# Kernel optimization log

Measured on AMD Instinct MI355X. Metric: run time of the kernel, lower is better.

## Reference

```python
import jax, jax.numpy as jnp
import numpy as np

K = 9            # kernel_size * dilation
ALPHA = 0.2      # LeakyReLU slope in GAT attention
LRELU = 0.01     # Grapher.layer1 default LeakyReLU slope
EPS_NORM = 1e-12
BN_EPS = 1e-5
NEG_INF = -9e15


def setup_inputs() -> dict:
    key = jax.random.key(0)
    ks = jax.random.split(key, 9)
    B, C, H, W = 16, 64, 32, 32
    nheads, nhid = 4, 15
    return {
        "x": jax.random.normal(ks[0], (B, C, H, W), jnp.float32),
        "W_heads": jax.random.normal(ks[1], (nheads, C, nhid), jnp.float32) * 0.2,
        "a_heads": jax.random.normal(ks[2], (nheads, 2 * nhid, 1), jnp.float32) * 0.2,
        "W_out": jax.random.normal(ks[3], (nheads * nhid, C), jnp.float32) * 0.2,
        "a_out": jax.random.normal(ks[4], (2 * C, 1), jnp.float32) * 0.2,
        "conv_w": jax.random.normal(ks[5], (C, C), jnp.float32) * 0.1,
        "conv_b": jax.random.normal(ks[6], (C,), jnp.float32) * 0.1,
        "bn_gamma": jnp.ones((C,), jnp.float32),
        "bn_beta": jnp.zeros((C,), jnp.float32),
    }


def _gat_layer(h, adj, W, a, concat):
    # h: [B,N,Fin], W: [Fin,Fout], a: [2*Fout,1]
    Wh = h @ W                                   # [B,N,Fout]
    Fout = W.shape[1]
    f1 = Wh @ a[:Fout]                           # [B,N,1]  (a . Wh_i)
    f2 = Wh @ a[Fout:]                           # [B,N,1]  (a . Wh_j)
    e = jax.nn.leaky_relu(f1 + jnp.swapaxes(f2, 1, 2), ALPHA)  # [B,N,N]
    att = jnp.where(adj > 0, e, NEG_INF)
    att = jax.nn.softmax(att, axis=1)            # torch F.softmax(dim=1)
    hp = att @ Wh                                # [B,N,Fout]
    return jax.nn.elu(hp) if concat else hp


def reference(x, W_heads, a_heads, W_out, a_out, conv_w, conv_b, bn_gamma, bn_beta):
    B, C, H, W = x.shape
    N = H * W
    res = x
    xf = x.reshape(B, C, N)                      # [B,C,N]
    # F.normalize(p=2, dim=1)
    nrm = jnp.maximum(jnp.linalg.norm(xf, axis=1, keepdims=True), EPS_NORM)
    h = jnp.swapaxes(xf / nrm, 1, 2)             # [B,N,C]
    # KNN adjacency (built under no_grad in the original)
    hs = jax.lax.stop_gradient(h)
    sq = jnp.sum(hs * hs, axis=-1, keepdims=True)        # [B,N,1]
    dist = sq - 2.0 * (hs @ jnp.swapaxes(hs, 1, 2)) + jnp.swapaxes(sq, 1, 2)
    _, idx = jax.lax.top_k(-dist, K)                      # [B,N,K]
    adj = jnp.zeros((B, N, N), x.dtype).at[
        jnp.arange(B)[:, None, None], jnp.arange(N)[None, :, None], idx
    ].set(1.0)
    # 4-head GAT (dropout is identity in eval mode)
    heads = [_gat_layer(h, adj, W_heads[i], a_heads[i], True)
             for i in range(W_heads.shape[0])]
    hcat = jnp.concatenate(heads, axis=2)        # [B,N,60]
    out = jax.nn.elu(_gat_layer(hcat, adj, W_out, a_out, False))  # [B,N,C]
    y = jnp.swapaxes(out, 1, 2).reshape(B, C, H, W)
    y = jax.nn.leaky_relu(y, LRELU)
    # 1x1 conv + BatchNorm (eval: running_mean=0, running_var=1)
    y = jnp.einsum('bchw,oc->bohw', y, conv_w) + conv_b[None, :, None, None]
    y = y / jnp.sqrt(1.0 + BN_EPS) * bn_gamma[None, :, None, None] + bn_beta[None, :, None, None]
    return y + res
```

## Files before the change

### kernel.cpp

```cpp
#include <hip/hip_runtime.h>
#include <math.h>

#define NB 16
#define NC 64
#define NN 1024
#define NK 9
#define NH 4
#define NF 15

#define OFF_HN     0
#define OFF_SQV    1048576
#define OFF_IDX    1064960
#define OFF_DEN1   1212416
#define OFF_U1     1277952
#define OFF_DEN2   1278976
#define OFF_U2     1295360
#define OFF_F11    1296384
#define OFF_F21    1361920
#define OFF_F12    1427456
#define OFF_F22    1443840
#define OFF_E1     1460224
#define OFF_E2     2050048
#define OFF_WH1    2197504
#define OFF_HCAT   3246080
#define OFF_WH2    4294656
#define OFF_YTIL   5343232
#define ZERO_BASE  OFF_DEN1
#define ZERO_LEN   83968

__device__ __forceinline__ unsigned fkey(float x){
  unsigned b = __float_as_uint(x);
  return (b & 0x80000000u) ? ~b : (b | 0x80000000u);
}
__device__ __forceinline__ float eluf(float x){ return x > 0.f ? x : expm1f(x); }

__global__ __launch_bounds__(256) void k1_norm_wh(const float* __restrict__ x,
    const float* __restrict__ W_heads, const float* __restrict__ a_heads,
    float* __restrict__ hn, float* __restrict__ sqv, float* __restrict__ Wh1,
    float* __restrict__ f1, float* __restrict__ f2, float* __restrict__ ws){
  int t = blockIdx.x*256 + threadIdx.x;
  if (t < ZERO_LEN) ws[ZERO_BASE + t] = 0.f;
  if (t >= NB*NN) return;
  int b = t >> 10, n = t & 1023;
  const float* xb = x + b*NC*NN;
  float* hb = hn + b*NC*NN;
  float s = 0.f;
  #pragma unroll
  for (int c = 0; c < NC; c++){ float v = xb[c*NN + n]; s = fmaf(v, v, s); }
  float nrm = fmaxf(sqrtf(s), 1e-12f);
  float wh[NH][NF];
  #pragma unroll
  for (int hh = 0; hh < NH; hh++)
    #pragma unroll
    for (int f = 0; f < NF; f++) wh[hh][f] = 0.f;
  float s2 = 0.f;
  for (int c = 0; c < NC; c++){
    float v = xb[c*NN + n] / nrm;
    hb[c*NN + n] = v;
    s2 = fmaf(v, v, s2);
    #pragma unroll
    for (int hh = 0; hh < NH; hh++){
      const float* W = W_heads + (hh*NC + c)*NF;
      #pragma unroll
      for (int f = 0; f < NF; f++) wh[hh][f] = fmaf(v, W[f], wh[hh][f]);
    }
  }
  sqv[t] = s2;
  float* orow = Wh1 + ((size_t)(b*NN) + n)*64;
  #pragma unroll
  for (int hh = 0; hh < NH; hh++){
    const float* al = a_heads + hh*2*NF;
    float s1 = 0.f, sb = 0.f;
    #pragma unroll
    for (int f = 0; f < NF; f++){ s1 = fmaf(wh[hh][f], al[f], s1); sb = fmaf(wh[hh][f], al[NF+f], sb); }
    float4* o4 = (float4*)(orow + hh*16);
    o4[0] = make_float4(wh[hh][0], wh[hh][1], wh[hh][2], wh[hh][3]);
    o4[1] = make_float4(wh[hh][4], wh[hh][5], wh[hh][6], wh[hh][7]);
    o4[2] = make_float4(wh[hh][8], wh[hh][9], wh[hh][10], wh[hh][11]);
    o4[3] = make_float4(wh[hh][12], wh[hh][13], wh[hh][14], 0.f);
    int hb2 = hh*NB + b;
    f1[hb2*NN + n] = s1; f2[hb2*NN + n] = sb;
  }
}

#define LSTR 68
__global__ __launch_bounds__(256) void k2_knn(const float* __restrict__ hn,
    const float* __restrict__ sqv, const float* __restrict__ f1g, const float* __restrict__ f2g,
    int* __restrict__ idxb, float* __restrict__ e1, float* __restrict__ den1){
  __shared__ float As[64][LSTR];
  __shared__ float Bs[64][LSTR];
  __shared__ float Ds[64][LSTR];
  __shared__ float ssq[64], sjq[64];
  int b  = blockIdx.y;
  int i0 = blockIdx.x * 64;
  int tid = threadIdx.x;
  const float* hb = hn + b*NC*NN;
  #pragma unroll
  for (int k = 0; k < 4; k++){
    int idx4 = tid + k*256;
    int c = idx4 >> 4, q4 = (idx4 & 15) * 4;
    *(float4*)&As[c][q4] = *(const float4*)&hb[c*NN + i0 + q4];
  }
  if (tid < 64) ssq[tid] = sqv[b*NN + i0 + tid];
  int rg = tid >> 4, cg = tid & 15;
  int r  = tid >> 2, p  = tid & 3;
  unsigned long long s0=~0ull,s1=~0ull,s2k=~0ull,s3=~0ull,s4=~0ull,s5=~0ull,s6=~0ull,s7=~0ull,s8=~0ull;
  for (int jt = 0; jt < 16; jt++){
    int j0 = jt * 64;
    __syncthreads();
    #pragma unroll
    for (int k = 0; k < 4; k++){
      int idx4 = tid + k*256;
      int c = idx4 >> 4, q4 = (idx4 & 15) * 4;
      *(float4*)&Bs[c][q4] = *(const float4*)&hb[c*NN + j0 + q4];
    }
    if (tid < 64) sjq[tid] = sqv[b*NN + j0 + tid];
    __syncthreads();
    float acc[4][4];
    #pragma unroll
    for (int q = 0; q < 4; q++)
      #pragma unroll
      for (int jj = 0; jj < 4; jj++) acc[q][jj] = 0.f;
    #pragma unroll 4
    for (int c = 0; c < 64; c++){
      float4 a  = *(const float4*)&As[c][rg*4];
      float4 bb = *(const float4*)&Bs[c][cg*4];
      float av[4] = {a.x, a.y, a.z, a.w};
      float bv[4] = {bb.x, bb.y, bb.z, bb.w};
      #pragma unroll
      for (int q = 0; q < 4; q++)
        #pragma unroll
        for (int jj = 0; jj < 4; jj++) acc[q][jj] = fmaf(av[q], bv[jj], acc[q][jj]);
    }
    #pragma unroll
    for (int q = 0; q < 4; q++){
      float si = ssq[rg*4+q];
      float4 o;
      o.x = (si - 2.f*acc[q][0]) + sjq[cg*4+0];
      o.y = (si - 2.f*acc[q][1]) + sjq[cg*4+1];
      o.z = (si - 2.f*acc[q][2]) + sjq[cg*4+2];
      o.w = (si - 2.f*acc[q][3]) + sjq[cg*4+3];
      *(float4*)&Ds[rg*4+q][cg*4] = o;
    }
    __syncthreads();
    #pragma unroll
    for (int m = 0; m < 4; m++){
      float4 v = *(const float4*)&Ds[r][p*16 + m*4];
      float vv[4] = {v.x, v.y, v.z, v.w};
      #pragma unroll
      for (int q = 0; q < 4; q++){
        unsigned long long kk = ((unsigned long long)fkey(vv[q]) << 32)
                              | (unsigned)(j0 + p*16 + m*4 + q);
        if (kk < s8){
          s8 = kk;
          unsigned long long tt;
          if (s8 < s7){ tt=s7; s7=s8; s8=tt; }
          if (s7 < s6){ tt=s6; s6=s7; s7=tt; }
          if (s6 < s5){ tt=s5; s5=s6; s6=tt; }
          if (s5 < s4){ tt=s4; s4=s5; s5=tt; }
          if (s4 < s3){ tt=s3; s3=s4; s4=tt; }
          if (s3 < s2k){ tt=s2k; s2k=s3; s3=tt; }
          if (s2k < s1){ tt=s1; s1=s2k; s2k=tt; }
          if (s1 < s0){ tt=s0; s0=s1; s1=tt; }
        }
      }
    }
  }
  int i = i0 + r;
  int hbh = p*NB + b;
  float f1v = f1g[hbh*NN + i];
  unsigned long long h = s0;
  #pragma unroll
  for (int round = 0; round < NK; round++){
    unsigned long long g = h;
    unsigned long long o1 = __shfl_xor(g, 1); g = o1 < g ? o1 : g;
    unsigned long long o2 = __shfl_xor(g, 2); g = o2 < g ? o2 : g;
    if (h == g){
      s0=s1; s1=s2k; s2k=s3; s3=s4; s4=s5; s5=s6; s6=s7; s7=s8; s8=~0ull; h=s0;
    }
    int j = (int)(g & 0xFFFFFFFFu);
    if (p == 0) idxb[((size_t)(b*NN) + i)*NK + round] = j;
    float e = f1v + f2g[hbh*NN + j];
    e = e >= 0.f ? e : 0.2f*e;
    e1[((size_t)(hbh*NN) + i)*NK + round] = e;
    atomicAdd(den1 + hbh*NN + j, expf(e));
  }
}

__global__ __launch_bounds__(256) void k4b_u1(const float* __restrict__ denom1,
                       const float* __restrict__ Wh1, float* __restrict__ u1){
  int t = blockIdx.x*256 + threadIdx.x;
  if (denom1[t] != 0.f) return;
  int hb = t >> 10, j = t & 1023;
  int hh = hb >> 4, b = hb & 15;
  const float* w = Wh1 + ((size_t)(b*NN) + j)*64 + hh*16;
  for (int f = 0; f < NF; f++) atomicAdd(u1 + hb*16 + f, w[f] * (1.f/1024.f));
}

__global__ __launch_bounds__(256) void k5_hp1(const int* __restrict__ idxb, const float* __restrict__ e1,
    const float* __restrict__ denom1, const float* __restrict__ Wh1,
    const float* __restrict__ u1, float* __restrict__ hcat){
  int wave = threadIdx.x >> 6, lane = threadIdx.x & 63;
  int t = blockIdx.x*4 + wave;
  int b = t >> 10, i = t & 1023;
  int hh = lane >> 4, f = lane & 15;
  int hb = hh*NB + b;
  float acc = u1[hb*16 + f];
  const int* jp = idxb + (size_t)t*NK;
  const float* ep = e1 + (size_t)(hb*NN + i)*NK;
  const float* dn = denom1 + hb*NN;
  const float* wbase = Wh1 + ((size_t)(b*NN))*64;
  #pragma unroll 3
  for (int k = 0; k < NK; k++){
    int j = jp[k];
    float att = expf(ep[k]) / dn[j];
    acc = fmaf(att, wbase[(size_t)j*64 + lane], acc);
  }
  if (f < NF) hcat[((size_t)(b*NN) + i)*64 + hh*NF + f] = eluf(acc);
}

__global__ __launch_bounds__(256) void k7_wh2(const float* __restrict__ hcat,
    const float* __restrict__ W_out, const float* __restrict__ a_out,
    float* __restrict__ Wh2, float* __restrict__ f1, float* __restrict__ f2){
  __shared__ float hcl[64][65];
  __shared__ float p1[4][64], p2[4][64];
  int b = blockIdx.y, n0 = blockIdx.x*64;
  for (int t = threadIdx.x; t < 4096; t += 256){
    int nl = t >> 6, c = t & 63;
    hcl[nl][c] = hcat[(size_t)((b*NN) + n0 + nl)*64 + c];
  }
  __syncthreads();
  int nl = threadIdx.x & 63;
  int wv = threadIdx.x >> 6;
  int og = __builtin_amdgcn_readfirstlane(wv * 16);
  float z[16];
  #pragma unroll
  for (int m = 0; m < 16; m++) z[m] = 0.f;
  for (int c = 0; c < 60; c++){
    float yv = hcl[nl][c];
    #pragma unroll
    for (int m = 0; m < 16; m++) z[m] = fmaf(yv, W_out[c*64 + og + m], z[m]);
  }
  int n = n0 + nl;
  float* o = Wh2 + ((size_t)(b*NN) + n)*64 + og;
  #pragma unroll
  for (int m = 0; m < 16; m += 4) *(float4*)&o[m] = make_float4(z[m],z[m+1],z[m+2],z[m+3]);
  float s1 = 0.f, s2 = 0.f;
  #pragma unroll
  for (int m = 0; m < 16; m++){ s1 = fmaf(z[m], a_out[og+m], s1); s2 = fmaf(z[m], a_out[64+og+m], s2); }
  p1[wv][nl] = s1; p2[wv][nl] = s2;
  __syncthreads();
  if (threadIdx.x < 64){
    f1[b*NN + n0 + threadIdx.x] = p1[0][threadIdx.x] + p1[1][threadIdx.x] + p1[2][threadIdx.x] + p1[3][threadIdx.x];
    f2[b*NN + n0 + threadIdx.x] = p2[0][threadIdx.x] + p2[1][threadIdx.x] + p2[2][threadIdx.x] + p2[3][threadIdx.x];
  }
}

__global__ __launch_bounds__(256) void k8_edge2(const int* __restrict__ idxb, const float* __restrict__ f1,
                         const float* __restrict__ f2, float* __restrict__ e2,
                         float* __restrict__ denom2){
  int t = blockIdx.x*256 + threadIdx.x;
  int bi = t / 9;
  int b = bi >> 10;
  int j = idxb[t];
  float e = f1[bi] + f2[b*NN + j];
  e = e >= 0.f ? e : 0.2f*e;
  e2[t] = e;
  atomicAdd(denom2 + b*NN + j, expf(e));
}

__global__ __launch_bounds__(256) void k8b_u2(const float* __restrict__ denom2,
                       const float* __restrict__ Wh2, float* __restrict__ u2){
  int t = blockIdx.x*256 + threadIdx.x;
  if (denom2[t] != 0.f) return;
  int b = t >> 10;
  const float* w = Wh2 + (size_t)t*64;
  for (int f = 0; f < 64; f++) atomicAdd(u2 + b*64 + f, w[f] * (1.f/1024.f));
}

__global__ __launch_bounds__(256) void k9_hp2(const int* __restrict__ idxb, const float* __restrict__ e2,
    const float* __restrict__ denom2, const float* __restrict__ Wh2,
    const float* __restrict__ u2, float* __restrict__ ytil){
  int wave = threadIdx.x >> 6, lane = threadIdx.x & 63;
  int t = blockIdx.x*4 + wave;
  int b = t >> 10;
  float acc = u2[b*64 + lane];
  const int* jp = idxb + (size_t)t*NK;
  const float* ep = e2 + (size_t)t*NK;
  const float* dn = denom2 + b*NN;
  const float* wbase = Wh2 + ((size_t)(b*NN))*64;
  #pragma unroll 3
  for (int k = 0; k < NK; k++){
    int j = jp[k];
    float att = expf(ep[k]) / dn[j];
    acc = fmaf(att, wbase[(size_t)j*64 + lane], acc);
  }
  float v = eluf(acc);
  ytil[(size_t)t*64 + lane] = v >= 0.f ? v : 0.01f*v;
}

__global__ __launch_bounds__(256) void k11_conv(const float* __restrict__ ytil,
    const float* __restrict__ conv_w, const float* __restrict__ conv_b,
    const float* __restrict__ bn_g, const float* __restrict__ bn_b,
    const float* __restrict__ x, float* __restrict__ out){
  __shared__ float yt[64][65];
  int b = blockIdx.y, n0 = blockIdx.x*64;
  for (int t = threadIdx.x; t < 4096; t += 256){
    int nl = t >> 6, c = t & 63;
    yt[nl][c] = ytil[(size_t)((b*NN) + n0 + nl)*64 + c];
  }
  __syncthreads();
  int nl = threadIdx.x & 63;
  int og = __builtin_amdgcn_readfirstlane((int)(threadIdx.x >> 6) * 16);
  float z[16];
  #pragma unroll
  for (int m = 0; m < 16; m++) z[m] = 0.f;
  for (int c = 0; c < 64; c++){
    float yv = yt[nl][c];
    #pragma unroll
    for (int m = 0; m < 16; m++) z[m] = fmaf(yv, conv_w[(og+m)*64 + c], z[m]);
  }
  const float scbn = 1.f / sqrtf(1.f + 1e-5f);
  #pragma unroll
  for (int m = 0; m < 16; m++){
    int o = og + m;
    size_t oi = ((size_t)(b*64 + o))*NN + n0 + nl;
    out[oi] = fmaf(z[m] + conv_b[o], bn_g[o]*scbn, bn_b[o]) + x[oi];
  }
}

extern "C" void kernel_launch(void* const* d_in, const int* in_sizes, int n_in,
                              void* d_out, int out_size, void* d_ws, size_t ws_size,
                              hipStream_t stream){
  (void)in_sizes; (void)n_in; (void)out_size; (void)ws_size;
  const float* x       = (const float*)d_in[0];
  const float* W_heads = (const float*)d_in[1];
  const float* a_heads = (const float*)d_in[2];
  const float* W_out   = (const float*)d_in[3];
  const float* a_out   = (const float*)d_in[4];
  const float* conv_w  = (const float*)d_in[5];
  const float* conv_b  = (const float*)d_in[6];
  const float* bn_g    = (const float*)d_in[7];
  const float* bn_b    = (const float*)d_in[8];
  float* ws  = (float*)d_ws;
  float* out = (float*)d_out;

  float* hn   = ws + OFF_HN;
  float* sqv  = ws + OFF_SQV;
  int*   idxb = (int*)(ws + OFF_IDX);
  float* den1 = ws + OFF_DEN1;
  float* u1   = ws + OFF_U1;
  float* den2 = ws + OFF_DEN2;
  float* u2   = ws + OFF_U2;
  float* f11  = ws + OFF_F11;
  float* f21  = ws + OFF_F21;
  float* f12  = ws + OFF_F12;
  float* f22  = ws + OFF_F22;
  float* e1   = ws + OFF_E1;
  float* e2   = ws + OFF_E2;
  float* Wh1  = ws + OFF_WH1;
  float* hcat = ws + OFF_HCAT;
  float* Wh2  = ws + OFF_WH2;
  float* ytil = ws + OFF_YTIL;

  k1_norm_wh<<<dim3(328), dim3(256), 0, stream>>>(x, W_heads, a_heads, hn, sqv, Wh1, f11, f21, ws);
  k2_knn<<<dim3(16,16), dim3(256), 0, stream>>>(hn, sqv, f11, f21, idxb, e1, den1);
  k4b_u1<<<dim3(256), dim3(256), 0, stream>>>(den1, Wh1, u1);
  k5_hp1<<<dim3(4096), dim3(256), 0, stream>>>(idxb, e1, den1, Wh1, u1, hcat);
  k7_wh2<<<dim3(16,16), dim3(256), 0, stream>>>(hcat, W_out, a_out, Wh2, f12, f22);
  k8_edge2<<<dim3(576), dim3(256), 0, stream>>>(idxb, f12, f22, e2, den2);
  k8b_u2<<<dim3(64), dim3(256), 0, stream>>>(den2, Wh2, u2);
  k9_hp2<<<dim3(4096), dim3(256), 0, stream>>>(idxb, e2, den2, Wh2, u2, ytil);
  k11_conv<<<dim3(16,16), dim3(256), 0, stream>>>(ytil, conv_w, conv_b, bn_g, bn_b, x, out);
}
```

Before: 284.4 us.

## Split KNN top-k across column quarters and merge candidates in a second kernel

The KNN distance/top-k kernel previously launched only 256 blocks, each scanning all 1024 columns. It now splits the column range into 4 quarters via blockIdx.z (1024 blocks), and each block writes its 9 local candidates to a workspace buffer. A new merge kernel reduces the 36 candidates per row to the final top-9, then computes the attention edge scores and denominators. This raises GPU occupancy on the dominant kernel at the cost of an extra launch and candidate-buffer traffic.

```diff
diff --git a/kernel.cpp b/kernel.cpp
--- a/kernel.cpp
+++ b/kernel.cpp
@@ -25,6 +25,7 @@
 #define OFF_HCAT   3246080
 #define OFF_WH2    4294656
 #define OFF_YTIL   5343232
+#define OFF_CAND   6391808
 #define ZERO_BASE  OFF_DEN1
 #define ZERO_LEN   83968
 
@@ -84,15 +85,15 @@
 }
 
 #define LSTR 68
-__global__ __launch_bounds__(256) void k2_knn(const float* __restrict__ hn,
-    const float* __restrict__ sqv, const float* __restrict__ f1g, const float* __restrict__ f2g,
-    int* __restrict__ idxb, float* __restrict__ e1, float* __restrict__ den1){
+__global__ __launch_bounds__(256) void k2cand(const float* __restrict__ hn,
+    const float* __restrict__ sqv, unsigned long long* __restrict__ cand){
   __shared__ float As[64][LSTR];
   __shared__ float Bs[64][LSTR];
   __shared__ float Ds[64][LSTR];
   __shared__ float ssq[64], sjq[64];
+  int i0 = blockIdx.x * 64;
   int b  = blockIdx.y;
-  int i0 = blockIdx.x * 64;
+  int jq = blockIdx.z;
   int tid = threadIdx.x;
   const float* hb = hn + b*NC*NN;
   #pragma unroll
@@ -105,8 +106,8 @@
   int rg = tid >> 4, cg = tid & 15;
   int r  = tid >> 2, p  = tid & 3;
   unsigned long long s0=~0ull,s1=~0ull,s2k=~0ull,s3=~0ull,s4=~0ull,s5=~0ull,s6=~0ull,s7=~0ull,s8=~0ull;
-  for (int jt = 0; jt < 16; jt++){
-    int j0 = jt * 64;
+  for (int jst = 0; jst < 4; jst++){
+    int j0 = jq*256 + jst*64;
     __syncthreads();
     #pragma unroll
     for (int k = 0; k < 4; k++){
@@ -167,8 +168,7 @@
     }
   }
   int i = i0 + r;
-  int hbh = p*NB + b;
-  float f1v = f1g[hbh*NN + i];
+  unsigned long long* cp = cand + ((size_t)(b*NN) + i)*36 + jq*9;
   unsigned long long h = s0;
   #pragma unroll
   for (int round = 0; round < NK; round++){
@@ -178,12 +178,53 @@
     if (h == g){
       s0=s1; s1=s2k; s2k=s3; s3=s4; s4=s5; s5=s6; s6=s7; s7=s8; s8=~0ull; h=s0;
     }
-    int j = (int)(g & 0xFFFFFFFFu);
-    if (p == 0) idxb[((size_t)(b*NN) + i)*NK + round] = j;
-    float e = f1v + f2g[hbh*NN + j];
-    e = e >= 0.f ? e : 0.2f*e;
-    e1[((size_t)(hbh*NN) + i)*NK + round] = e;
-    atomicAdd(den1 + hbh*NN + j, expf(e));
+    if (p == 0) cp[round] = g;
+  }
+}
+
+__global__ __launch_bounds__(256) void k2merge(const unsigned long long* __restrict__ cand,
+    const float* __restrict__ f1g, const float* __restrict__ f2g,
+    int* __restrict__ idxb, float* __restrict__ e1, float* __restrict__ den1){
+  int t = blockIdx.x*256 + threadIdx.x;
+  int b = t >> 10, i = t & 1023;
+  const unsigned long long* cp = cand + (size_t)t*36;
+  unsigned long long s0=~0ull,s1=~0ull,s2k=~0ull,s3=~0ull,s4=~0ull,s5=~0ull,s6=~0ull,s7=~0ull,s8=~0ull;
+  #pragma unroll
+  for (int m = 0; m < 36; m++){
+    unsigned long long kk = cp[m];
+    if (kk < s8){
+      s8 = kk;
+      unsigned long long tt;
+      if (s8 < s7){ tt=s7; s7=s8; s8=tt; }
+      if (s7 < s6){ tt=s6; s6=s7; s7=tt; }
+      if (s6 < s5){ tt=s5; s5=s6; s6=tt; }
+      if (s5 < s4){ tt=s4; s4=s5; s5=tt; }
+      if (s4 < s3){ tt=s3; s3=s4; s4=tt; }
+      if (s3 < s2k){ tt=s2k; s2k=s3; s3=tt; }
+      if (s2k < s1){ tt=s1; s1=s2k; s2k=tt; }
+      if (s1 < s0){ tt=s0; s0=s1; s1=tt; }
+    }
+  }
+  int jj[NK];
+  jj[0]=(int)(s0&0xFFFFFFFFu); jj[1]=(int)(s1&0xFFFFFFFFu); jj[2]=(int)(s2k&0xFFFFFFFFu);
+  jj[3]=(int)(s3&0xFFFFFFFFu); jj[4]=(int)(s4&0xFFFFFFFFu); jj[5]=(int)(s5&0xFFFFFFFFu);
+  jj[6]=(int)(s6&0xFFFFFFFFu); jj[7]=(int)(s7&0xFFFFFFFFu); jj[8]=(int)(s8&0xFFFFFFFFu);
+  int* op = idxb + (size_t)t*NK;
+  #pragma unroll
+  for (int k = 0; k < NK; k++) op[k] = jj[k];
+  #pragma unroll
+  for (int hh = 0; hh < NH; hh++){
+    int hb = hh*NB + b;
+    float f1v = f1g[hb*NN + i];
+    float* ep = e1 + ((size_t)(hb*NN) + i)*NK;
+    #pragma unroll
+    for (int k = 0; k < NK; k++){
+      int j = jj[k];
+      float e = f1v + f2g[hb*NN + j];
+      e = e >= 0.f ? e : 0.2f*e;
+      ep[k] = e;
+      atomicAdd(den1 + hb*NN + j, expf(e));
+    }
   }
 }
 
@@ -362,9 +403,11 @@
   float* hcat = ws + OFF_HCAT;
   float* Wh2  = ws + OFF_WH2;
   float* ytil = ws + OFF_YTIL;
+  unsigned long long* cand = (unsigned long long*)(ws + OFF_CAND);
 
   k1_norm_wh<<<dim3(328), dim3(256), 0, stream>>>(x, W_heads, a_heads, hn, sqv, Wh1, f11, f21, ws);
-  k2_knn<<<dim3(16,16), dim3(256), 0, stream>>>(hn, sqv, f11, f21, idxb, e1, den1);
+  k2cand<<<dim3(16,16,4), dim3(256), 0, stream>>>(hn, sqv, cand);
+  k2merge<<<dim3(64), dim3(256), 0, stream>>>(cand, f11, f21, idxb, e1, den1);
   k4b_u1<<<dim3(256), dim3(256), 0, stream>>>(den1, Wh1, u1);
   k5_hp1<<<dim3(4096), dim3(256), 0, stream>>>(idxb, e1, den1, Wh1, u1, hcat);
   k7_wh2<<<dim3(16,16), dim3(256), 0, stream>>>(hcat, W_out, a_out, Wh2, f12, f22);
```

Result: faster. 262.9 us (-7.6%).
